# Kernel tuning notes

Hardware: AMD Instinct MI355X
Metric: run time of the kernel (lower is better)

Reference implementation:

```python
import jax, jax.numpy as jnp
import numpy as np

DIM = 1024
H = 16          # num query heads
KV = 8          # num kv heads
HD = DIM // H   # head_dim = 64
B, P = 8, 1024


def setup_inputs() -> dict:
    key = jax.random.key(0)
    ks = jax.random.split(key, 6)
    s = 0.02
    return {
        "x": jax.random.normal(ks[0], (B, P, DIM), dtype=jnp.float32),
        "Wq": jax.random.normal(ks[1], (DIM, DIM), dtype=jnp.float32) * s,
        "Wk": jax.random.normal(ks[2], (KV * HD, DIM), dtype=jnp.float32) * s,
        "Wv": jax.random.normal(ks[3], (KV * HD, DIM), dtype=jnp.float32) * s,
        "Wp": jax.random.normal(ks[4], (DIM, DIM), dtype=jnp.float32) * s,
        "bp": jax.random.normal(ks[5], (DIM,), dtype=jnp.float32) * s,
    }


def _q_allocations(k):
    # k: (B, KV, P, HD). k_norms: frobenius norm over (P, HD), summed over batch.
    kn = jnp.sqrt(jnp.sum(k * k, axis=(2, 3))).sum(axis=0)  # (KV,)
    kn = (kn - kn.min()) / (kn.max() - kn.min())
    alloc = jnp.round(kn / kn.sum() * H).astype(jnp.int32)   # (KV,)
    # fix up so alloc.sum() == H (mirrors the torch while-loops)
    alloc = jax.lax.while_loop(lambda a: a.sum() > H,
                               lambda a: a.at[jnp.argmax(a)].add(-1), alloc)
    alloc = jax.lax.while_loop(lambda a: a.sum() < H,
                               lambda a: a.at[jnp.argmin(a)].add(1), alloc)
    return alloc


def reference(x, Wq, Wk, Wv, Wp, bp):
    Bx, Px, C = x.shape
    scale = HD ** -0.5
    q = (x @ Wq.T).reshape(Bx, Px, H, HD).transpose(0, 2, 1, 3) * scale  # (B,H,P,HD)
    k = (x @ Wk.T).reshape(Bx, Px, KV, HD).transpose(0, 2, 1, 3)         # (B,KV,P,HD)
    v = (x @ Wv.T).reshape(Bx, Px, KV, HD).transpose(0, 2, 1, 3)

    alloc = _q_allocations(k)  # (KV,) sums to H
    # query head h belongs to kv group i where cumsum[i-1] <= h < cumsum[i].
    # Equivalent to torch.split(q, alloc) + per-group attention, because the
    # per-group softmax over keys is independent per query head.
    kv_idx = jnp.searchsorted(jnp.cumsum(alloc), jnp.arange(H), side='right')
    k_g = jnp.take(k, kv_idx, axis=1)  # (B,H,P,HD)
    v_g = jnp.take(v, kv_idx, axis=1)

    scores = jnp.einsum('bhqd,bhkd->bhqk', q, k_g)
    weights = jax.nn.softmax(scores, axis=-1)
    out = jnp.einsum('bhqk,bhkd->bhqd', weights, v_g)  # (B,H,P,HD)
    out = out.transpose(0, 2, 1, 3).reshape(Bx, Px, C)
    return out @ Wp.T + bp
```

## Files before the change

kernel.cpp:

```cpp
#include <hip/hip_runtime.h>
#include <stdint.h>


typedef float f32x4 __attribute__((ext_vector_type(4)));
typedef short s16x8 __attribute__((ext_vector_type(8)));
typedef short s16x4 __attribute__((ext_vector_type(4)));
typedef int   i32x4 __attribute__((ext_vector_type(4)));

__device__ __forceinline__ unsigned short f2bf(float f) {
  unsigned int u = __builtin_bit_cast(unsigned int, f);
  u = (u + 0x7FFFu + ((u >> 16) & 1u)) >> 16;
  return (unsigned short)u;
}
__device__ __forceinline__ float bf2f(unsigned short h) {
  unsigned int u = ((unsigned int)h) << 16;
  return __builtin_bit_cast(float, u);
}

__device__ __forceinline__ unsigned int pk_bf16(float a, float b) {
#if __has_builtin(__builtin_amdgcn_cvt_pk_bf16_f32)
  auto v = __builtin_amdgcn_cvt_pk_bf16_f32(a, b);
  return __builtin_bit_cast(unsigned int, v);
#else
  unsigned int ua = __builtin_bit_cast(unsigned int, a);
  unsigned int ub = __builtin_bit_cast(unsigned int, b);
  ua += 0x7FFFu + ((ua >> 16) & 1u);
  ub += 0x7FFFu + ((ub >> 16) & 1u);
#if __has_builtin(__builtin_amdgcn_perm)
  return __builtin_amdgcn_perm(ub, ua, 0x07060302);
#else
  return (ua >> 16) | (ub & 0xFFFF0000u);
#endif
#endif
}

__device__ __forceinline__ float fast_exp2(float x) {
#if __has_builtin(__builtin_amdgcn_exp2f)
  return __builtin_amdgcn_exp2f(x);
#else
  return exp2f(x);
#endif
}

#if __has_builtin(__builtin_amdgcn_global_load_lds)
#define HAVE_GLL 1
typedef const __attribute__((address_space(1))) void* gas_ptr;
typedef __attribute__((address_space(3))) void* las_ptr;
__device__ __forceinline__ void gll16(const void* g, void* l) {
  __builtin_amdgcn_global_load_lds((gas_ptr)g, (las_ptr)l, 16, 0, 0);
}
#endif

__global__ void convert_kernel(const float* __restrict__ x, const float* __restrict__ Wq,
                               const float* __restrict__ Wk, const float* __restrict__ Wv,
                               const float* __restrict__ Wp,
                               unsigned short* __restrict__ xb,
                               unsigned short* __restrict__ wqkv,
                               unsigned short* __restrict__ wpb) {
  const long i = ((long)blockIdx.x * 256 + threadIdx.x) * 4;
  const float* src; unsigned short* dst; long off; float scale = 1.0f;
  if (i < 8388608L)       { src = x;  dst = xb;             off = i;             }
  else if (i < 9437184L)  { src = Wq; dst = wqkv;           off = i - 8388608L;  scale = 0.18033688011112042f; }
  else if (i < 9961472L)  { src = Wk; dst = wqkv + 1048576; off = i - 9437184L;  }
  else if (i < 10485760L) { src = Wv; dst = wqkv + 1572864; off = i - 9961472L;  }
  else                    { src = Wp; dst = wpb;            off = i - 10485760L; }
  f32x4 v = *(const f32x4*)(src + off);
  s16x4 o;
  o[0] = (short)f2bf(v[0] * scale);
  o[1] = (short)f2bf(v[1] * scale);
  o[2] = (short)f2bf(v[2] * scale);
  o[3] = (short)f2bf(v[3] * scale);
  *(s16x4*)(dst + off) = o;
}

template<int N, bool OUT_BF16>
__global__ __launch_bounds__(256)
void gemm_bt(const unsigned short* __restrict__ A,
             const unsigned short* __restrict__ Bw,
             unsigned short* __restrict__ Cb,
             float* __restrict__ Cf,
             const float* __restrict__ bias) {
  __shared__ __align__(16) unsigned short As[8192];
  __shared__ __align__(16) unsigned short Bs[8192];
  constexpr int NB = N / 128;
  const int bm = blockIdx.x / NB, bn = blockIdx.x % NB;
  const int m0 = bm * 128, n0 = bn * 128;
  const int t = threadIdx.x;
  const int w = t >> 6, lane = t & 63, quad = lane >> 4, ln = lane & 15;
  const int wm = w & 1, wn = w >> 1;

  const int lrow = lane >> 3;
  const int lc8  = ((lane & 7) ^ lrow) << 3;
  const unsigned short* agl = A  + (m0 + w * 32 + lrow) * 1024 + lc8;
  const unsigned short* bgl = Bw + (n0 + w * 32 + lrow) * 1024 + lc8;

  f32x4 acc[4][4] = {};

  for (int k0 = 0; k0 < 1024; k0 += 64) {
    __syncthreads();
#ifdef HAVE_GLL
    #pragma unroll
    for (int c = 0; c < 4; ++c) {
      gll16(agl + k0 + c * 8192, &As[w * 2048 + c * 512]);
      gll16(bgl + k0 + c * 8192, &Bs[w * 2048 + c * 512]);
    }
#else
    i32x4 ra[4], rb[4];
    #pragma unroll
    for (int c = 0; c < 4; ++c) {
      ra[c] = *(const i32x4*)(agl + k0 + c * 8192);
      rb[c] = *(const i32x4*)(bgl + k0 + c * 8192);
    }
    #pragma unroll
    for (int c = 0; c < 4; ++c) {
      *(i32x4*)(&As[w * 2048 + c * 512 + lane * 8]) = ra[c];
      *(i32x4*)(&Bs[w * 2048 + c * 512 + lane * 8]) = rb[c];
    }
#endif
    __syncthreads();
    #pragma unroll
    for (int kc = 0; kc < 2; ++kc) {
      const int pcs = ((kc * 4 + quad) ^ (ln & 7)) << 3;
      s16x8 af[4], bf[4];
      #pragma unroll
      for (int i = 0; i < 4; ++i)
        af[i] = *(const s16x8*)(&As[(wm * 64 + i * 16 + ln) * 64 + pcs]);
      #pragma unroll
      for (int j = 0; j < 4; ++j)
        bf[j] = *(const s16x8*)(&Bs[(wn * 64 + j * 16 + ln) * 64 + pcs]);
      #pragma unroll
      for (int i = 0; i < 4; ++i)
        #pragma unroll
        for (int j = 0; j < 4; ++j)
          acc[i][j] = __builtin_amdgcn_mfma_f32_16x16x32_bf16(af[i], bf[j], acc[i][j], 0, 0, 0);
    }
  }

  #pragma unroll
  for (int j = 0; j < 4; ++j) {
    const int gn = n0 + wn * 64 + j * 16 + ln;
    float bv = 0.0f;
    if constexpr (!OUT_BF16) bv = bias[gn];
    #pragma unroll
    for (int i = 0; i < 4; ++i) {
      const int gm0 = m0 + wm * 64 + i * 16 + quad * 4;
      #pragma unroll
      for (int r = 0; r < 4; ++r) {
        float v = acc[i][j][r];
        if constexpr (OUT_BF16) Cb[(gm0 + r) * N + gn] = f2bf(v);
        else                    Cf[(gm0 + r) * N + gn] = v + bv;
      }
    }
  }
}

__global__ void sumsq_kernel(const unsigned short* __restrict__ qkv,
                             float* __restrict__ sumsq) {
  const int cell = blockIdx.x;
  const int b = cell >> 3, kv = cell & 7;
  const unsigned short* base = qkv + (long)b * 1024 * 2048 + 1024 + kv * 64;
  float s = 0.0f;
  for (int i = threadIdx.x * 4; i < 65536; i += 1024) {
    const int row = i >> 6, col = i & 63;
    s16x4 v4 = *(const s16x4*)(base + row * 2048 + col);
    #pragma unroll
    for (int j = 0; j < 4; ++j) {
      float f = bf2f((unsigned short)v4[j]);
      s += f * f;
    }
  }
  #pragma unroll
  for (int o = 32; o > 0; o >>= 1) s += __shfl_down(s, o);
  __shared__ float red[4];
  if ((threadIdx.x & 63) == 0) red[threadIdx.x >> 6] = s;
  __syncthreads();
  if (threadIdx.x == 0) sumsq[cell] = red[0] + red[1] + red[2] + red[3];
}

__global__ void alloc_kernel(const float* __restrict__ sumsq, int* __restrict__ kvidx) {
  if (threadIdx.x != 0) return;
  float kn[8];
  for (int kv = 0; kv < 8; ++kv) {
    float s = 0.0f;
    for (int b = 0; b < 8; ++b) s += sqrtf(sumsq[b * 8 + kv]);
    kn[kv] = s;
  }
  float mn = kn[0], mx = kn[0];
  for (int i = 1; i < 8; ++i) { mn = fminf(mn, kn[i]); mx = fmaxf(mx, kn[i]); }
  float tot = 0.0f;
  for (int i = 0; i < 8; ++i) { kn[i] = (kn[i] - mn) / (mx - mn); tot += kn[i]; }
  int a[8], sum = 0;
  for (int i = 0; i < 8; ++i) { a[i] = (int)rintf(kn[i] * 16.0f / tot); sum += a[i]; }
  while (sum > 16) {
    int im = 0;
    for (int i = 1; i < 8; ++i) if (a[i] > a[im]) im = i;
    a[im]--; sum--;
  }
  while (sum < 16) {
    int im = 0;
    for (int i = 1; i < 8; ++i) if (a[i] < a[im]) im = i;
    a[im]++; sum++;
  }
  int c[8], cum = 0;
  for (int i = 0; i < 8; ++i) { cum += a[i]; c[i] = cum; }
  for (int h = 0; h < 16; ++h) {
    int idx = 0;
    while (c[idx] <= h) idx++;
    kvidx[h] = idx;
  }
}

__global__ __launch_bounds__(256)
void attn_kernel(const unsigned short* __restrict__ qkv,
                 const int* __restrict__ kvidx,
                 unsigned short* __restrict__ att) {
  __shared__ __align__(16) unsigned short Ks[64][72];
  __shared__ __align__(16) unsigned short Vt[64][72];
  __shared__ __align__(16) float Pl[4][16][68];

  const int bid = blockIdx.x;
  const int h = bid & 15, qt = (bid >> 4) & 15, b = bid >> 8;
  const int kvi = kvidx[h];

  const int t = threadIdx.x, w = t >> 6, lane = t & 63, quad = lane >> 4, ln = lane & 15;

  const int qrow = b * 1024 + qt * 64 + w * 16 + ln;
  const unsigned short* qp = qkv + qrow * 2048 + h * 64 + quad * 8;
  const s16x8 qf0 = *(const s16x8*)(qp);
  const s16x8 qf1 = *(const s16x8*)(qp + 32);

  const int kkey = t >> 2, kd0 = (t & 3) << 4;
  const unsigned short* kbase = qkv + (b * 1024 + kkey) * 2048 + 1024 + kvi * 64 + kd0;
  const int kp = t & 31, vd0 = (t >> 5) << 3;
  const unsigned short* vbase = qkv + (b * 1024 + 2 * kp) * 2048 + 1536 + kvi * 64 + vd0;

  s16x8 ones;
  #pragma unroll
  for (int j = 0; j < 8; ++j) ones[j] = (short)0x3F80;

  f32x4 Oa[4] = {};
  f32x4 lacc = {};

  i32x4 ka0 = *(const i32x4*)(kbase);
  i32x4 ka1 = *(const i32x4*)(kbase + 8);
  s16x8 va0 = *(const s16x8*)(vbase);
  s16x8 va1 = *(const s16x8*)(vbase + 2048);

  for (int kt = 0; kt < 16; ++kt) {
    __syncthreads();
    *(i32x4*)(&Ks[kkey][kd0])     = ka0;
    *(i32x4*)(&Ks[kkey][kd0 + 8]) = ka1;
    #pragma unroll
    for (int i = 0; i < 8; ++i) {
      unsigned int pk = (unsigned int)(unsigned short)va0[i] |
                        ((unsigned int)(unsigned short)va1[i] << 16);
      *(unsigned int*)(&Vt[vd0 + i][2 * kp]) = pk;
    }
    __syncthreads();

    if (kt < 15) {
      const unsigned short* p = kbase + (kt + 1) * 131072;
      ka0 = *(const i32x4*)(p);
      ka1 = *(const i32x4*)(p + 8);
      const unsigned short* q = vbase + (kt + 1) * 131072;
      va0 = *(const s16x8*)(q);
      va1 = *(const s16x8*)(q + 2048);
    }

    f32x4 sacc[4] = {};
    #pragma unroll
    for (int ks = 0; ks < 4; ++ks) {
      s16x8 kf0 = *(const s16x8*)(&Ks[ks * 16 + ln][quad * 8]);
      s16x8 kf1 = *(const s16x8*)(&Ks[ks * 16 + ln][32 + quad * 8]);
      sacc[ks] = __builtin_amdgcn_mfma_f32_16x16x32_bf16(qf0, kf0, sacc[ks], 0, 0, 0);
      sacc[ks] = __builtin_amdgcn_mfma_f32_16x16x32_bf16(qf1, kf1, sacc[ks], 0, 0, 0);
    }

    #pragma unroll
    for (int ks = 0; ks < 4; ++ks)
      #pragma unroll
      for (int r = 0; r < 4; ++r)
        Pl[w][quad * 4 + r][ks * 16 + ln] = fast_exp2(sacc[ks][r]);
    __asm__ volatile("s_waitcnt lgkmcnt(0)" ::: "memory");

    #pragma unroll
    for (int kc = 0; kc < 2; ++kc) {
      f32x4 pa = *(const f32x4*)(&Pl[w][ln][kc * 32 + quad * 8]);
      f32x4 pb = *(const f32x4*)(&Pl[w][ln][kc * 32 + quad * 8 + 4]);
      unsigned int u0 = pk_bf16(pa[0], pa[1]);
      unsigned int u1 = pk_bf16(pa[2], pa[3]);
      unsigned int u2 = pk_bf16(pb[0], pb[1]);
      unsigned int u3 = pk_bf16(pb[2], pb[3]);
      i32x4 pfi; pfi[0] = (int)u0; pfi[1] = (int)u1; pfi[2] = (int)u2; pfi[3] = (int)u3;
      s16x8 pf = __builtin_bit_cast(s16x8, pfi);
      #pragma unroll
      for (int ds = 0; ds < 4; ++ds) {
        s16x8 vf = *(const s16x8*)(&Vt[ds * 16 + ln][kc * 32 + quad * 8]);
        Oa[ds] = __builtin_amdgcn_mfma_f32_16x16x32_bf16(pf, vf, Oa[ds], 0, 0, 0);
      }
      lacc = __builtin_amdgcn_mfma_f32_16x16x32_bf16(pf, ones, lacc, 0, 0, 0);
    }
  }

  float inv[4];
  #pragma unroll
  for (int r = 0; r < 4; ++r)
#if __has_builtin(__builtin_amdgcn_rcpf)
    inv[r] = __builtin_amdgcn_rcpf(lacc[r]);
#else
    inv[r] = 1.0f / lacc[r];
#endif

  const int orow = b * 1024 + qt * 64 + w * 16 + quad * 4;
  #pragma unroll
  for (int ds = 0; ds < 4; ++ds)
    #pragma unroll
    for (int r = 0; r < 4; ++r)
      att[(orow + r) * 1024 + h * 64 + ds * 16 + ln] = f2bf(Oa[ds][r] * inv[r]);
}

extern "C" void kernel_launch(void* const* d_in, const int* in_sizes, int n_in,
                              void* d_out, int out_size, void* d_ws, size_t ws_size,
                              hipStream_t stream) {
  const float* x  = (const float*)d_in[0];
  const float* Wq = (const float*)d_in[1];
  const float* Wk = (const float*)d_in[2];
  const float* Wv = (const float*)d_in[3];
  const float* Wp = (const float*)d_in[4];
  const float* bp = (const float*)d_in[5];

  char* ws = (char*)d_ws;
  unsigned short* xb   = (unsigned short*)(ws);
  unsigned short* wqkv = (unsigned short*)(ws + 16777216);
  unsigned short* wpb  = (unsigned short*)(ws + 20971520);
  unsigned short* qkv  = (unsigned short*)(ws + 23068672);
  float*          sums = (float*)(ws + 56623104);
  int*            kvix = (int*)(ws + 56623360);
  unsigned short* att  = xb;

  convert_kernel<<<11264, 256, 0, stream>>>(x, Wq, Wk, Wv, Wp, xb, wqkv, wpb);
  gemm_bt<2048, true><<<1024, 256, 0, stream>>>(xb, wqkv, qkv, nullptr, nullptr);
  sumsq_kernel<<<64, 256, 0, stream>>>(qkv, sums);
  alloc_kernel<<<1, 64, 0, stream>>>(sums, kvix);
  attn_kernel<<<2048, 256, 0, stream>>>(qkv, kvix, att);
  gemm_bt<1024, false><<<512, 256, 0, stream>>>(att, wpb, nullptr, (float*)d_out, bp);
}
```

Measured before the change: 259.0 us.

## Fuse K-norm reduction into QKV GEMM, inline allocation, double query tile in attention

Computes the per-batch, per-KV-head K sum of squares in the QKV GEMM epilogue using fp32 accumulators and atomics. The allocation logic moves into each attention block, which removes two small kernel launches and one re-read of K. The attention kernel now handles 128 queries per block, reusing each K/V tile for two query subtiles. It loads K into LDS with global_load_lds into a swizzled layout and stores P as packed bf16 instead of fp32 to cut LDS traffic. The trade-offs are more registers per thread and sums that now come from fp32 values rather than bf16-rounded ones, with atomic ordering nondeterminism.

```diff
diff --git a/kernel.cpp b/kernel.cpp
--- a/kernel.cpp
+++ b/kernel.cpp
@@ -34,6 +34,14 @@
 #endif
 }
 
+__device__ __forceinline__ unsigned int perm_half(unsigned int hi, unsigned int lo, int takeHi) {
+#if __has_builtin(__builtin_amdgcn_perm)
+  return __builtin_amdgcn_perm(hi, lo, takeHi ? 0x07060302u : 0x05040100u);
+#else
+  return takeHi ? ((lo >> 16) | (hi & 0xFFFF0000u)) : ((lo & 0xFFFFu) | (hi << 16));
+#endif
+}
+
 __device__ __forceinline__ float fast_exp2(float x) {
 #if __has_builtin(__builtin_amdgcn_exp2f)
   return __builtin_amdgcn_exp2f(x);
@@ -56,7 +64,9 @@
                                const float* __restrict__ Wp,
                                unsigned short* __restrict__ xb,
                                unsigned short* __restrict__ wqkv,
-                               unsigned short* __restrict__ wpb) {
+                               unsigned short* __restrict__ wpb,
+                               float* __restrict__ sums) {
+  if (blockIdx.x == 0 && threadIdx.x < 64) sums[threadIdx.x] = 0.0f;
   const long i = ((long)blockIdx.x * 256 + threadIdx.x) * 4;
   const float* src; unsigned short* dst; long off; float scale = 1.0f;
   if (i < 8388608L)       { src = x;  dst = xb;             off = i;             }
@@ -73,13 +83,14 @@
   *(s16x4*)(dst + off) = o;
 }
 
-template<int N, bool OUT_BF16>
+template<int N, bool OUT_BF16, bool DO_SUMSQ>
 __global__ __launch_bounds__(256)
 void gemm_bt(const unsigned short* __restrict__ A,
              const unsigned short* __restrict__ Bw,
              unsigned short* __restrict__ Cb,
              float* __restrict__ Cf,
-             const float* __restrict__ bias) {
+             const float* __restrict__ bias,
+             float* __restrict__ sums) {
   __shared__ __align__(16) unsigned short As[8192];
   __shared__ __align__(16) unsigned short Bs[8192];
   constexpr int NB = N / 128;
@@ -136,6 +147,23 @@
     }
   }
 
+  if constexpr (DO_SUMSQ) {
+    if (bn >= 8 && bn < 12) {
+      float ss = 0.0f;
+      #pragma unroll
+      for (int i = 0; i < 4; ++i)
+        #pragma unroll
+        for (int j = 0; j < 4; ++j)
+          #pragma unroll
+          for (int r = 0; r < 4; ++r)
+            ss += acc[i][j][r] * acc[i][j][r];
+      #pragma unroll
+      for (int off = 1; off < 64; off <<= 1) ss += __shfl_xor(ss, off);
+      if (lane == 0)
+        atomicAdd(&sums[(m0 >> 10) * 8 + (bn - 8) * 2 + wn], ss);
+    }
+  }
+
   #pragma unroll
   for (int j = 0; j < 4; ++j) {
     const int gn = n0 + wn * 64 + j * 16 + ln;
@@ -154,83 +182,64 @@
   }
 }
 
-__global__ void sumsq_kernel(const unsigned short* __restrict__ qkv,
-                             float* __restrict__ sumsq) {
-  const int cell = blockIdx.x;
-  const int b = cell >> 3, kv = cell & 7;
-  const unsigned short* base = qkv + (long)b * 1024 * 2048 + 1024 + kv * 64;
-  float s = 0.0f;
-  for (int i = threadIdx.x * 4; i < 65536; i += 1024) {
-    const int row = i >> 6, col = i & 63;
-    s16x4 v4 = *(const s16x4*)(base + row * 2048 + col);
-    #pragma unroll
-    for (int j = 0; j < 4; ++j) {
-      float f = bf2f((unsigned short)v4[j]);
-      s += f * f;
-    }
-  }
+__global__ __launch_bounds__(256, 4)
+void attn_kernel(const unsigned short* __restrict__ qkv,
+                 const float* __restrict__ sums,
+                 unsigned short* __restrict__ att) {
+  __shared__ __align__(16) unsigned short Ks[4096];
+  __shared__ __align__(16) unsigned short Vt[64][72];
+  __shared__ __align__(16) unsigned int  Plb[4][32][36];
+  __shared__ int kvs;
+
+  const int bid = blockIdx.x;
+  const int h = bid & 15, qt = (bid >> 4) & 7, b = bid >> 7;
+  const int t = threadIdx.x, w = t >> 6, lane = t & 63, quad = lane >> 4, ln = lane & 15;
+
+  if (t == 0) {
+    float kn[8];
+    for (int kv = 0; kv < 8; ++kv) {
+      float s = 0.0f;
+      for (int bb = 0; bb < 8; ++bb) s += sqrtf(sums[bb * 8 + kv]);
+      kn[kv] = s;
+    }
+    float mn = kn[0], mx = kn[0];
+    for (int i = 1; i < 8; ++i) { mn = fminf(mn, kn[i]); mx = fmaxf(mx, kn[i]); }
+    float tot = 0.0f;
+    for (int i = 0; i < 8; ++i) { kn[i] = (kn[i] - mn) / (mx - mn); tot += kn[i]; }
+    int a[8], sum = 0;
+    for (int i = 0; i < 8; ++i) { a[i] = (int)rintf(kn[i] * 16.0f / tot); sum += a[i]; }
+    while (sum > 16) {
+      int im = 0;
+      for (int i = 1; i < 8; ++i) if (a[i] > a[im]) im = i;
+      a[im]--; sum--;
+    }
+    while (sum < 16) {
+      int im = 0;
+      for (int i = 1; i < 8; ++i) if (a[i] < a[im]) im = i;
+      a[im]++; sum++;
+    }
+    int cum = 0, idx = 0, c[8];
+    for (int i = 0; i < 8; ++i) { cum += a[i]; c[i] = cum; }
+    while (c[idx] <= h) idx++;
+    kvs = idx;
+  }
+  __syncthreads();
+  const int kvi = kvs;
+
+  s16x8 qf[2][2];
   #pragma unroll
-  for (int o = 32; o > 0; o >>= 1) s += __shfl_down(s, o);
-  __shared__ float red[4];
-  if ((threadIdx.x & 63) == 0) red[threadIdx.x >> 6] = s;
-  __syncthreads();
-  if (threadIdx.x == 0) sumsq[cell] = red[0] + red[1] + red[2] + red[3];
-}
-
-__global__ void alloc_kernel(const float* __restrict__ sumsq, int* __restrict__ kvidx) {
-  if (threadIdx.x != 0) return;
-  float kn[8];
-  for (int kv = 0; kv < 8; ++kv) {
-    float s = 0.0f;
-    for (int b = 0; b < 8; ++b) s += sqrtf(sumsq[b * 8 + kv]);
-    kn[kv] = s;
-  }
-  float mn = kn[0], mx = kn[0];
-  for (int i = 1; i < 8; ++i) { mn = fminf(mn, kn[i]); mx = fmaxf(mx, kn[i]); }
-  float tot = 0.0f;
-  for (int i = 0; i < 8; ++i) { kn[i] = (kn[i] - mn) / (mx - mn); tot += kn[i]; }
-  int a[8], sum = 0;
-  for (int i = 0; i < 8; ++i) { a[i] = (int)rintf(kn[i] * 16.0f / tot); sum += a[i]; }
-  while (sum > 16) {
-    int im = 0;
-    for (int i = 1; i < 8; ++i) if (a[i] > a[im]) im = i;
-    a[im]--; sum--;
-  }
-  while (sum < 16) {
-    int im = 0;
-    for (int i = 1; i < 8; ++i) if (a[i] < a[im]) im = i;
-    a[im]++; sum++;
-  }
-  int c[8], cum = 0;
-  for (int i = 0; i < 8; ++i) { cum += a[i]; c[i] = cum; }
-  for (int h = 0; h < 16; ++h) {
-    int idx = 0;
-    while (c[idx] <= h) idx++;
-    kvidx[h] = idx;
-  }
-}
-
-__global__ __launch_bounds__(256)
-void attn_kernel(const unsigned short* __restrict__ qkv,
-                 const int* __restrict__ kvidx,
-                 unsigned short* __restrict__ att) {
-  __shared__ __align__(16) unsigned short Ks[64][72];
-  __shared__ __align__(16) unsigned short Vt[64][72];
-  __shared__ __align__(16) float Pl[4][16][68];
-
-  const int bid = blockIdx.x;
-  const int h = bid & 15, qt = (bid >> 4) & 15, b = bid >> 8;
-  const int kvi = kvidx[h];
-
-  const int t = threadIdx.x, w = t >> 6, lane = t & 63, quad = lane >> 4, ln = lane & 15;
-
-  const int qrow = b * 1024 + qt * 64 + w * 16 + ln;
-  const unsigned short* qp = qkv + qrow * 2048 + h * 64 + quad * 8;
-  const s16x8 qf0 = *(const s16x8*)(qp);
-  const s16x8 qf1 = *(const s16x8*)(qp + 32);
-
-  const int kkey = t >> 2, kd0 = (t & 3) << 4;
-  const unsigned short* kbase = qkv + (b * 1024 + kkey) * 2048 + 1024 + kvi * 64 + kd0;
+  for (int s = 0; s < 2; ++s) {
+    const unsigned short* qp = qkv + (b * 1024 + qt * 128 + s * 64 + w * 16 + ln) * 2048
+                               + h * 64 + quad * 8;
+    qf[s][0] = *(const s16x8*)(qp);
+    qf[s][1] = *(const s16x8*)(qp + 32);
+  }
+
+  const int lc8 = ((lane & 7) ^ (lane >> 3)) << 3;
+  const unsigned short* kglA = qkv + (b * 1024 + w * 16 + (lane >> 3)) * 2048
+                               + 1024 + kvi * 64 + lc8;
+  const unsigned short* kglB = kglA + 8 * 2048;
+
   const int kp = t & 31, vd0 = (t >> 5) << 3;
   const unsigned short* vbase = qkv + (b * 1024 + 2 * kp) * 2048 + 1536 + kvi * 64 + vd0;
 
@@ -238,18 +247,23 @@
   #pragma unroll
   for (int j = 0; j < 8; ++j) ones[j] = (short)0x3F80;
 
-  f32x4 Oa[4] = {};
-  f32x4 lacc = {};
-
-  i32x4 ka0 = *(const i32x4*)(kbase);
-  i32x4 ka1 = *(const i32x4*)(kbase + 8);
+  f32x4 Oa[2][4] = {};
+  f32x4 lacc[2] = {};
+
   s16x8 va0 = *(const s16x8*)(vbase);
   s16x8 va1 = *(const s16x8*)(vbase + 2048);
 
   for (int kt = 0; kt < 16; ++kt) {
     __syncthreads();
-    *(i32x4*)(&Ks[kkey][kd0])     = ka0;
-    *(i32x4*)(&Ks[kkey][kd0 + 8]) = ka1;
+#ifdef HAVE_GLL
+    gll16(kglA + kt * 131072, Ks + w * 1024);
+    gll16(kglB + kt * 131072, Ks + w * 1024 + 512);
+#else
+    i32x4 t0 = *(const i32x4*)(kglA + kt * 131072);
+    i32x4 t1 = *(const i32x4*)(kglB + kt * 131072);
+    *(i32x4*)(Ks + w * 1024 + lane * 8) = t0;
+    *(i32x4*)(Ks + w * 1024 + 512 + lane * 8) = t1;
+#endif
     #pragma unroll
     for (int i = 0; i < 8; ++i) {
       unsigned int pk = (unsigned int)(unsigned short)va0[i] |
@@ -259,64 +273,72 @@
     __syncthreads();
 
     if (kt < 15) {
-      const unsigned short* p = kbase + (kt + 1) * 131072;
-      ka0 = *(const i32x4*)(p);
-      ka1 = *(const i32x4*)(p + 8);
       const unsigned short* q = vbase + (kt + 1) * 131072;
       va0 = *(const s16x8*)(q);
       va1 = *(const s16x8*)(q + 2048);
     }
 
-    f32x4 sacc[4] = {};
-    #pragma unroll
-    for (int ks = 0; ks < 4; ++ks) {
-      s16x8 kf0 = *(const s16x8*)(&Ks[ks * 16 + ln][quad * 8]);
-      s16x8 kf1 = *(const s16x8*)(&Ks[ks * 16 + ln][32 + quad * 8]);
-      sacc[ks] = __builtin_amdgcn_mfma_f32_16x16x32_bf16(qf0, kf0, sacc[ks], 0, 0, 0);
-      sacc[ks] = __builtin_amdgcn_mfma_f32_16x16x32_bf16(qf1, kf1, sacc[ks], 0, 0, 0);
-    }
-
-    #pragma unroll
-    for (int ks = 0; ks < 4; ++ks)
-      #pragma unroll
-      for (int r = 0; r < 4; ++r)
-        Pl[w][quad * 4 + r][ks * 16 + ln] = fast_exp2(sacc[ks][r]);
+    #pragma unroll
+    for (int s = 0; s < 2; ++s) {
+      f32x4 sacc[4] = {};
+      #pragma unroll
+      for (int ks = 0; ks < 4; ++ks) {
+        const int r0 = (ks * 16 + ln) * 64;
+        s16x8 kf0 = *(const s16x8*)(Ks + r0 + (((quad    ) ^ (ln & 7)) << 3));
+        s16x8 kf1 = *(const s16x8*)(Ks + r0 + (((quad + 4) ^ (ln & 7)) << 3));
+        sacc[ks] = __builtin_amdgcn_mfma_f32_16x16x32_bf16(qf[s][0], kf0, sacc[ks], 0, 0, 0);
+        sacc[ks] = __builtin_amdgcn_mfma_f32_16x16x32_bf16(qf[s][1], kf1, sacc[ks], 0, 0, 0);
+      }
+      #pragma unroll
+      for (int r = 0; r < 4; ++r) {
+        unsigned int d0 = pk_bf16(fast_exp2(sacc[0][r]), fast_exp2(sacc[1][r]));
+        unsigned int d1 = pk_bf16(fast_exp2(sacc[2][r]), fast_exp2(sacc[3][r]));
+        unsigned int* pr = &Plb[w][s * 16 + quad * 4 + r][0];
+        pr[ln]      = d0;
+        pr[ln + 16] = d1;
+      }
+    }
     __asm__ volatile("s_waitcnt lgkmcnt(0)" ::: "memory");
 
     #pragma unroll
     for (int kc = 0; kc < 2; ++kc) {
-      f32x4 pa = *(const f32x4*)(&Pl[w][ln][kc * 32 + quad * 8]);
-      f32x4 pb = *(const f32x4*)(&Pl[w][ln][kc * 32 + quad * 8 + 4]);
-      unsigned int u0 = pk_bf16(pa[0], pa[1]);
-      unsigned int u1 = pk_bf16(pa[2], pa[3]);
-      unsigned int u2 = pk_bf16(pb[0], pb[1]);
-      unsigned int u3 = pk_bf16(pb[2], pb[3]);
-      i32x4 pfi; pfi[0] = (int)u0; pfi[1] = (int)u1; pfi[2] = (int)u2; pfi[3] = (int)u3;
-      s16x8 pf = __builtin_bit_cast(s16x8, pfi);
+      s16x8 pf[2];
+      #pragma unroll
+      for (int s = 0; s < 2; ++s) {
+        const unsigned int* base = &Plb[w][s * 16 + ln][kc * 16 + (quad & 1) * 8];
+        i32x4 u0 = *(const i32x4*)(base);
+        i32x4 u1 = *(const i32x4*)(base + 4);
+        const int th = quad >> 1;
+        i32x4 pp;
+        pp[0] = (int)perm_half((unsigned)u0[1], (unsigned)u0[0], th);
+        pp[1] = (int)perm_half((unsigned)u0[3], (unsigned)u0[2], th);
+        pp[2] = (int)perm_half((unsigned)u1[1], (unsigned)u1[0], th);
+        pp[3] = (int)perm_half((unsigned)u1[3], (unsigned)u1[2], th);
+        pf[s] = __builtin_bit_cast(s16x8, pp);
+      }
       #pragma unroll
       for (int ds = 0; ds < 4; ++ds) {
         s16x8 vf = *(const s16x8*)(&Vt[ds * 16 + ln][kc * 32 + quad * 8]);
-        Oa[ds] = __builtin_amdgcn_mfma_f32_16x16x32_bf16(pf, vf, Oa[ds], 0, 0, 0);
-      }
-      lacc = __builtin_amdgcn_mfma_f32_16x16x32_bf16(pf, ones, lacc, 0, 0, 0);
-    }
-  }
-
-  float inv[4];
+        Oa[0][ds] = __builtin_amdgcn_mfma_f32_16x16x32_bf16(pf[0], vf, Oa[0][ds], 0, 0, 0);
+        Oa[1][ds] = __builtin_amdgcn_mfma_f32_16x16x32_bf16(pf[1], vf, Oa[1][ds], 0, 0, 0);
+      }
+      lacc[0] = __builtin_amdgcn_mfma_f32_16x16x32_bf16(pf[0], ones, lacc[0], 0, 0, 0);
+      lacc[1] = __builtin_amdgcn_mfma_f32_16x16x32_bf16(pf[1], ones, lacc[1], 0, 0, 0);
+    }
+  }
+
   #pragma unroll
-  for (int r = 0; r < 4; ++r)
-#if __has_builtin(__builtin_amdgcn_rcpf)
-    inv[r] = __builtin_amdgcn_rcpf(lacc[r]);
-#else
-    inv[r] = 1.0f / lacc[r];
-#endif
-
-  const int orow = b * 1024 + qt * 64 + w * 16 + quad * 4;
-  #pragma unroll
-  for (int ds = 0; ds < 4; ++ds)
-    #pragma unroll
-    for (int r = 0; r < 4; ++r)
-      att[(orow + r) * 1024 + h * 64 + ds * 16 + ln] = f2bf(Oa[ds][r] * inv[r]);
+  for (int s = 0; s < 2; ++s) {
+    float inv[4];
+    #pragma unroll
+    for (int r = 0; r < 4; ++r) inv[r] = 1.0f / lacc[s][r];
+    const int orow = b * 1024 + qt * 128 + s * 64 + w * 16 + quad * 4;
+    #pragma unroll
+    for (int ds = 0; ds < 4; ++ds)
+      #pragma unroll
+      for (int r = 0; r < 4; ++r)
+        att[(orow + r) * 1024 + h * 64 + ds * 16 + ln] = f2bf(Oa[s][ds][r] * inv[r]);
+  }
 }
 
 extern "C" void kernel_launch(void* const* d_in, const int* in_sizes, int n_in,
@@ -335,13 +357,10 @@
   unsigned short* wpb  = (unsigned short*)(ws + 20971520);
   unsigned short* qkv  = (unsigned short*)(ws + 23068672);
   float*          sums = (float*)(ws + 56623104);
-  int*            kvix = (int*)(ws + 56623360);
   unsigned short* att  = xb;
 
-  convert_kernel<<<11264, 256, 0, stream>>>(x, Wq, Wk, Wv, Wp, xb, wqkv, wpb);
-  gemm_bt<2048, true><<<1024, 256, 0, stream>>>(xb, wqkv, qkv, nullptr, nullptr);
-  sumsq_kernel<<<64, 256, 0, stream>>>(qkv, sums);
-  alloc_kernel<<<1, 64, 0, stream>>>(sums, kvix);
-  attn_kernel<<<2048, 256, 0, stream>>>(qkv, kvix, att);
-  gemm_bt<1024, false><<<512, 256, 0, stream>>>(att, wpb, nullptr, (float*)d_out, bp);
-}
+  convert_kernel<<<11264, 256, 0, stream>>>(x, Wq, Wk, Wv, Wp, xb, wqkv, wpb, sums);
+  gemm_bt<2048, true, true><<<1024, 256, 0, stream>>>(xb, wqkv, qkv, nullptr, nullptr, sums);
+  attn_kernel<<<1024, 256, 0, stream>>>(qkv, sums, att);
+  gemm_bt<1024, false, false><<<512, 256, 0, stream>>>(att, wpb, nullptr, (float*)d_out, bp, nullptr);
+}
```

Measured after the change: 219.9 us. -15.1%, faster.
